# Kernel tuning notes

Measured on AMD Instinct MI355X. Metric: run time of the kernel, lower is better.

## Reference

```python
import jax, jax.numpy as jnp
from jax import lax
import numpy as np

B, T, R, U = 32, 32, 256, 4  # batch, exposures, recon size, upscale (2**(lambda_scale_factor-1))
YS = R // U                  # yt_img_size = 64


def setup_inputs() -> dict:
    key = jax.random.key(0)
    k = jax.random.split(key, 6)
    yt = jax.random.normal(k[0], (B, T, YS, YS), dtype=jnp.float32)
    Ht = jax.random.normal(k[1], (T, R, R), dtype=jnp.float32) * 0.1
    W1 = jax.random.normal(k[2], (32, 1, 3, 3), dtype=jnp.float32) * 0.1
    b1 = jnp.zeros((32,), dtype=jnp.float32)
    W2 = jax.random.normal(k[3], (1, 32, 3, 3), dtype=jnp.float32) * 0.1
    b2 = jnp.zeros((1,), dtype=jnp.float32)
    return {"yt": yt, "Ht": Ht, "W1": W1, "b1": b1, "W2": W2, "b2": b2}


def _conv(x, w, b):
    # NCHW / OIHW, stride 1, SAME padding
    y = lax.conv_general_dilated(x, w, window_strides=(1, 1), padding="SAME",
                                 dimension_numbers=("NCHW", "OIHW", "NCHW"))
    return y + b[None, :, None, None]


def reference(yt, Ht, W1, b1, W2, b2):
    # Structured A^T @ yt without materializing the (R^2, T*YS^2) sparse matrix:
    # out[b,p,q] = sum_t Ht[t,p,q] * yt[b,t,p//U,q//U]
    yt_up = jnp.repeat(jnp.repeat(yt, U, axis=2), U, axis=3)      # (B,T,R,R) nearest upsample
    x = jnp.einsum("btpq,tpq->bpq", yt_up, Ht)[:, None]            # (B,1,R,R)
    # upsample_postproc_block: Conv(1->32,3x3) -> ReLU -> Conv(32->1,3x3)
    x = jax.nn.relu(_conv(x, W1, b1))
    x = _conv(x, W2, b2)
    return x
```

## Files before the change

kernel.cpp:

```cpp
#include <hip/hip_runtime.h>

#define R 256
#define T 32

#define TROWS 8
#define TCOLS 32
#define XROWS 12
#define XCOLS 36
#define HR 10
#define HC 34
#define HSTR 36
#define CP 360
#define NPX (HR * HC)
#define NSLOT 6

__global__ __launch_bounds__(256) void einsum_kernel(
    const float* __restrict__ yt, const float* __restrict__ Ht,
    float* __restrict__ x) {
  const int idx = blockIdx.x;
  const int rh  = idx >> 8;
  const int yy  = (idx & 255) >> 2;
  const int bq  = idx & 3;
  const int b0  = bq * 8;
  const int tid = threadIdx.x;
  const int q   = tid;
  const int q4  = q >> 2;

  __shared__ float yts[8 * 32 * 64];

#pragma unroll
  for (int i = 0; i < 16; ++i) {
    int f4  = tid + i * 256;
    int b_l = f4 >> 9;
    int t   = (f4 >> 4) & 31;
    int xx4 = f4 & 15;
    float4 v = *(const float4*)(yt + (((size_t)(b0 + b_l) * T + t) * 64 + yy) * 64 + xx4 * 4);
    *(float4*)(yts + f4 * 4) = v;
  }
  __syncthreads();

  for (int rr = 0; rr < 2; ++rr) {
    const int p = yy * 4 + rh * 2 + rr;
    float ht[T];
#pragma unroll
    for (int t = 0; t < T; ++t) ht[t] = Ht[((size_t)t * R + p) * R + q];

#pragma unroll
    for (int b_l = 0; b_l < 8; ++b_l) {
      const float* ys = yts + b_l * 2048 + q4;
      float acc = 0.f;
#pragma unroll
      for (int t = 0; t < T; ++t) acc += ht[t] * ys[t * 64];
      x[((size_t)(b0 + b_l) * R + p) * R + q] = acc;
    }
  }
}

template <bool EDGE>
__device__ __forceinline__ void conv_body(
    const float (&patch)[NSLOT][9], bool slot5, const bool (&oob)[NSLOT],
    const int (&sw)[NSLOT], float* hs,
    const float* __restrict__ W1, const float* __restrict__ b1,
    const float* __restrict__ W2, int cl, int hboff, float (&acc)[4][4]) {
  for (int cg = 0; cg < 8; ++cg) {
    float w2[9];
#pragma unroll
    for (int k = 0; k < 9; ++k) w2[k] = W2[(cg * 4 + cl) * 9 + k];

#pragma unroll
    for (int c = 0; c < 4; ++c) {
      const int ch = cg * 4 + c;
      const float bias = b1[ch];
#pragma unroll
      for (int it = 0; it < NSLOT; ++it) {
        if (it < 5 || slot5) {
          float h = bias;
#pragma unroll
          for (int k = 0; k < 9; ++k) h += W1[ch * 9 + k] * patch[it][k];
          h = fmaxf(h, 0.f);
          if (EDGE) {
            if (oob[it]) h = 0.f;
          }
          hs[c * CP + sw[it]] = h;
        }
      }
    }
    __syncthreads();

#pragma unroll
    for (int j = 0; j < 6; ++j) {
      float4 v4 = *(const float4*)(hs + hboff + j * HSTR);
      float2 v2 = *(const float2*)(hs + hboff + j * HSTR + 4);
      float v[6] = {v4.x, v4.y, v4.z, v4.w, v2.x, v2.y};
#pragma unroll
      for (int dy = 0; dy < 3; ++dy) {
        int ai = j - dy;
        if (ai >= 0 && ai < 4) {
#pragma unroll
          for (int dx = 0; dx < 3; ++dx) {
            const float w = w2[dy * 3 + dx];
#pragma unroll
            for (int px = 0; px < 4; ++px) acc[ai][px] += w * v[px + dx];
          }
        }
      }
    }
    __syncthreads();
  }
}

__global__ __launch_bounds__(64) void conv_fused_kernel(
    const float* __restrict__ x, const float* __restrict__ W1,
    const float* __restrict__ b1, const float* __restrict__ W2,
    const float* __restrict__ b2, float* __restrict__ out) {
  __shared__ float xs[XROWS * XCOLS];
  __shared__ float hs[4 * CP];

  const int tid  = threadIdx.x;
  const int b    = blockIdx.x >> 8;
  const int tile = blockIdx.x & 255;
  const int oy0  = (tile >> 3) * TROWS;
  const int ox0  = (tile & 7) * TCOLS;
  const float* xb = x + (size_t)b * R * R;

  for (int i = tid; i < XROWS * XCOLS; i += 64) {
    int rr = i / XCOLS, cc = i % XCOLS;
    int gy = oy0 - 2 + rr, gx = ox0 - 2 + cc;
    float v = 0.f;
    if (gy >= 0 && gy < R && gx >= 0 && gx < R) v = xb[gy * R + gx];
    xs[i] = v;
  }
  __syncthreads();

  float patch[NSLOT][9];
  int  sw[NSLOT];
  bool oob[NSLOT];
  const bool slot5 = (tid < NPX - 5 * 64);
#pragma unroll
  for (int it = 0; it < NSLOT; ++it) {
    int px = tid + it * 64;
    bool act = (it < 5) || slot5;
    int hy = act ? (px / HC) : 0;
    int hx = act ? (px % HC) : 0;
    sw[it] = hy * HSTR + hx;
    int ghy = oy0 - 1 + hy, ghx = ox0 - 1 + hx;
    oob[it] = !((ghy >= 0) & (ghy < R) & (ghx >= 0) & (ghx < R));
#pragma unroll
    for (int ky = 0; ky < 3; ++ky)
#pragma unroll
      for (int kx = 0; kx < 3; ++kx)
        patch[it][ky * 3 + kx] = act ? xs[(hy + ky) * XCOLS + hx + kx] : 0.f;
  }

  const int g  = tid & 7;
  const int cl = (tid >> 3) & 3;
  const int rh = tid >> 5;
  const int r0 = 4 * rh;

  float acc[4][4];
#pragma unroll
  for (int ai = 0; ai < 4; ++ai)
#pragma unroll
    for (int px = 0; px < 4; ++px) acc[ai][px] = 0.f;

  const int hboff = cl * CP + r0 * HSTR + 4 * g;

  const bool edge = (oy0 == 0) | (oy0 == R - TROWS) | (ox0 == 0) | (ox0 == R - TCOLS);
  if (edge)
    conv_body<true>(patch, slot5, oob, sw, hs, W1, b1, W2, cl, hboff, acc);
  else
    conv_body<false>(patch, slot5, oob, sw, hs, W1, b1, W2, cl, hboff, acc);

  const float bias2 = b2[0];
#pragma unroll
  for (int ai = 0; ai < 4; ++ai)
#pragma unroll
    for (int px = 0; px < 4; ++px) {
      float v = acc[ai][px];
      v += __shfl_xor(v, 8);
      v += __shfl_xor(v, 16);
      acc[ai][px] = v;
    }
  if (cl == 0) {
#pragma unroll
    for (int ai = 0; ai < 4; ++ai) {
      float4 o = {acc[ai][0] + bias2, acc[ai][1] + bias2,
                  acc[ai][2] + bias2, acc[ai][3] + bias2};
      *(float4*)(out + (size_t)b * R * R + (oy0 + r0 + ai) * R + ox0 + 4 * g) = o;
    }
  }
}

extern "C" void kernel_launch(void* const* d_in, const int* in_sizes, int n_in,
                              void* d_out, int out_size, void* d_ws, size_t ws_size,
                              hipStream_t stream) {
  const float* yt = (const float*)d_in[0];
  const float* Ht = (const float*)d_in[1];
  const float* W1 = (const float*)d_in[2];
  const float* b1 = (const float*)d_in[3];
  const float* W2 = (const float*)d_in[4];
  const float* b2 = (const float*)d_in[5];
  float* outp = (float*)d_out;
  float* x    = (float*)d_ws;

  einsum_kernel<<<512, 256, 0, stream>>>(yt, Ht, x);
  conv_fused_kernel<<<8192, 64, 0, stream>>>(x, W1, b1, W2, b2, outp);
}
```

Baseline: 145.9 us.

## Pack four independent wave tiles per block with wave-local LDS fences

The conv kernel now runs four waves per 256-thread block. Each wave owns its own 8x32 output tile and its own LDS slice for the hidden activations. Block-wide barriers are replaced by an lgkmcnt wait, because only the same wave reads and writes its slice. The shared xs staging buffer is removed, so each lane reads its 3x3 input patches straight from global memory (with bounds checks on edge tiles), relying on cache instead of an explicit stage. This cuts barrier cost and the block count. In exchange it adds redundant global loads and depends on the wave-synchronous LDS ordering being correct.

```diff
diff --git a/kernel.cpp b/kernel.cpp
--- a/kernel.cpp
+++ b/kernel.cpp
@@ -5,14 +5,15 @@
 
 #define TROWS 8
 #define TCOLS 32
-#define XROWS 12
-#define XCOLS 36
 #define HR 10
 #define HC 34
 #define HSTR 36
 #define CP 360
+#define WSLICE (4 * CP)
 #define NPX (HR * HC)
 #define NSLOT 6
+
+#define WAVE_FENCE() asm volatile("s_waitcnt lgkmcnt(0)" ::: "memory")
 
 __global__ __launch_bounds__(256) void einsum_kernel(
     const float* __restrict__ yt, const float* __restrict__ Ht,
@@ -85,7 +86,7 @@
         }
       }
     }
-    __syncthreads();
+    WAVE_FENCE();
 
 #pragma unroll
     for (int j = 0; j < 6; ++j) {
@@ -105,56 +106,51 @@
         }
       }
     }
-    __syncthreads();
-  }
-}
-
-__global__ __launch_bounds__(64) void conv_fused_kernel(
-    const float* __restrict__ x, const float* __restrict__ W1,
-    const float* __restrict__ b1, const float* __restrict__ W2,
-    const float* __restrict__ b2, float* __restrict__ out) {
-  __shared__ float xs[XROWS * XCOLS];
-  __shared__ float hs[4 * CP];
-
-  const int tid  = threadIdx.x;
-  const int b    = blockIdx.x >> 8;
-  const int tile = blockIdx.x & 255;
-  const int oy0  = (tile >> 3) * TROWS;
-  const int ox0  = (tile & 7) * TCOLS;
-  const float* xb = x + (size_t)b * R * R;
-
-  for (int i = tid; i < XROWS * XCOLS; i += 64) {
-    int rr = i / XCOLS, cc = i % XCOLS;
-    int gy = oy0 - 2 + rr, gx = ox0 - 2 + cc;
-    float v = 0.f;
-    if (gy >= 0 && gy < R && gx >= 0 && gx < R) v = xb[gy * R + gx];
-    xs[i] = v;
-  }
-  __syncthreads();
-
+    WAVE_FENCE();
+  }
+}
+
+template <bool EDGE>
+__device__ __forceinline__ void conv_tile(
+    const float* __restrict__ xb, int ty0, int ox0, int lane, float* hsw,
+    const float* __restrict__ W1, const float* __restrict__ b1,
+    const float* __restrict__ W2, const float* __restrict__ b2,
+    float* __restrict__ outp) {
   float patch[NSLOT][9];
   int  sw[NSLOT];
   bool oob[NSLOT];
-  const bool slot5 = (tid < NPX - 5 * 64);
+  const bool slot5 = (lane < NPX - 5 * 64);
 #pragma unroll
   for (int it = 0; it < NSLOT; ++it) {
-    int px = tid + it * 64;
+    int px = lane + it * 64;
     bool act = (it < 5) || slot5;
     int hy = act ? (px / HC) : 0;
     int hx = act ? (px % HC) : 0;
     sw[it] = hy * HSTR + hx;
-    int ghy = oy0 - 1 + hy, ghx = ox0 - 1 + hx;
+    int ghy = ty0 - 1 + hy, ghx = ox0 - 1 + hx;
     oob[it] = !((ghy >= 0) & (ghy < R) & (ghx >= 0) & (ghx < R));
-#pragma unroll
-    for (int ky = 0; ky < 3; ++ky)
-#pragma unroll
-      for (int kx = 0; kx < 3; ++kx)
-        patch[it][ky * 3 + kx] = act ? xs[(hy + ky) * XCOLS + hx + kx] : 0.f;
-  }
-
-  const int g  = tid & 7;
-  const int cl = (tid >> 3) & 3;
-  const int rh = tid >> 5;
+    if (EDGE) {
+#pragma unroll
+      for (int ky = 0; ky < 3; ++ky)
+#pragma unroll
+        for (int kx = 0; kx < 3; ++kx) {
+          int gy = ty0 - 2 + hy + ky, gx = ox0 - 2 + hx + kx;
+          bool ok = (gy >= 0) & (gy < R) & (gx >= 0) & (gx < R);
+          patch[it][ky * 3 + kx] = ok ? xb[gy * R + gx] : 0.f;
+        }
+    } else {
+      const float* gp = xb + (ty0 - 2 + hy) * R + (ox0 - 2 + hx);
+#pragma unroll
+      for (int ky = 0; ky < 3; ++ky)
+#pragma unroll
+        for (int kx = 0; kx < 3; ++kx)
+          patch[it][ky * 3 + kx] = gp[ky * R + kx];
+    }
+  }
+
+  const int g  = lane & 7;
+  const int cl = (lane >> 3) & 3;
+  const int rh = lane >> 5;
   const int r0 = 4 * rh;
 
   float acc[4][4];
@@ -165,11 +161,7 @@
 
   const int hboff = cl * CP + r0 * HSTR + 4 * g;
 
-  const bool edge = (oy0 == 0) | (oy0 == R - TROWS) | (ox0 == 0) | (ox0 == R - TCOLS);
-  if (edge)
-    conv_body<true>(patch, slot5, oob, sw, hs, W1, b1, W2, cl, hboff, acc);
-  else
-    conv_body<false>(patch, slot5, oob, sw, hs, W1, b1, W2, cl, hboff, acc);
+  conv_body<EDGE>(patch, slot5, oob, sw, hsw, W1, b1, W2, cl, hboff, acc);
 
   const float bias2 = b2[0];
 #pragma unroll
@@ -186,9 +178,33 @@
     for (int ai = 0; ai < 4; ++ai) {
       float4 o = {acc[ai][0] + bias2, acc[ai][1] + bias2,
                   acc[ai][2] + bias2, acc[ai][3] + bias2};
-      *(float4*)(out + (size_t)b * R * R + (oy0 + r0 + ai) * R + ox0 + 4 * g) = o;
-    }
-  }
+      *(float4*)(outp + (ty0 + r0 + ai) * R + ox0 + 4 * g) = o;
+    }
+  }
+}
+
+__global__ __launch_bounds__(256) void conv_fused_kernel(
+    const float* __restrict__ x, const float* __restrict__ W1,
+    const float* __restrict__ b1, const float* __restrict__ W2,
+    const float* __restrict__ b2, float* __restrict__ out) {
+  __shared__ float hs[4 * WSLICE];
+
+  const int tid  = threadIdx.x;
+  const int lane = tid & 63;
+  const int wv   = tid >> 6;
+  const int b    = blockIdx.x >> 6;
+  const int tile = blockIdx.x & 63;
+  const int ty0  = (tile >> 3) * 32 + wv * TROWS;
+  const int ox0  = (tile & 7) * TCOLS;
+  const float* xb   = x + (size_t)b * R * R;
+  float*       outp = out + (size_t)b * R * R;
+  float*       hsw  = hs + wv * WSLICE;
+
+  const bool edge = (ty0 == 0) | (ty0 == R - TROWS) | (ox0 == 0) | (ox0 == R - TCOLS);
+  if (edge)
+    conv_tile<true>(xb, ty0, ox0, lane, hsw, W1, b1, W2, b2, outp);
+  else
+    conv_tile<false>(xb, ty0, ox0, lane, hsw, W1, b1, W2, b2, outp);
 }
 
 extern "C" void kernel_launch(void* const* d_in, const int* in_sizes, int n_in,
@@ -204,5 +220,5 @@
   float* x    = (float*)d_ws;
 
   einsum_kernel<<<512, 256, 0, stream>>>(yt, Ht, x);
-  conv_fused_kernel<<<8192, 64, 0, stream>>>(x, W1, b1, W2, b2, outp);
-}
+  conv_fused_kernel<<<2048, 256, 0, stream>>>(x, W1, b1, W2, b2, outp);
+}
```

Measured after the change: 143.0 us. -2.0%, faster.
